# Kernel optimization log

Hardware: AMD Instinct MI355X
Metric: run time of the kernel (lower is better)

Reference implementation:

```python
import jax, jax.numpy as jnp
from jax import lax
import numpy as np

B, S, I, H = 128, 256, 1024, 1024


def setup_inputs() -> dict:
    key = jax.random.key(0)
    ks = jax.random.split(key, 9)
    scale = 1.0 / np.sqrt(I + H)  # ~ torch Linear default init scale
    mk_w = lambda k: jax.random.normal(k, (H, I + H), dtype=jnp.float32) * scale
    mk_b = lambda k: jax.random.normal(k, (H,), dtype=jnp.float32) * scale
    return {
        "x": jax.random.normal(ks[0], (B, S, I), dtype=jnp.float32),
        "Wf": mk_w(ks[1]), "bf": mk_b(ks[2]),
        "Wi": mk_w(ks[3]), "bi": mk_b(ks[4]),
        "Wc": mk_w(ks[5]), "bc": mk_b(ks[6]),
        "Wo": mk_w(ks[7]), "bo": mk_b(ks[8]),
    }


def reference(x, Wf, bf, Wi, bi, Wc, bc, Wo, bo):
    # x: [B, S, I]; weights: [H, I+H] acting on cat(h_t, x_t) (hidden first!)
    b, s, _ = x.shape
    h = Wf.shape[0]
    h0 = jnp.zeros((b, h), dtype=x.dtype)
    c0 = jnp.zeros((b, h), dtype=x.dtype)

    def step(carry, x_t):
        h_t, c_t = carry
        z = jnp.concatenate([h_t, x_t], axis=1)  # [B, H+I]
        f = jax.nn.sigmoid(z @ Wf.T + bf)
        i = jax.nn.sigmoid(z @ Wi.T + bi)
        g = jnp.tanh(z @ Wc.T + bc)
        c_new = c_t * f + i * g
        o = jax.nn.sigmoid(z @ Wo.T + bo)
        h_new = jnp.tanh(c_new) * o
        return (h_new, c_new), h_new

    _, hs = lax.scan(step, (h0, c0), jnp.swapaxes(x, 0, 1))  # hs: [S, B, H]
    return jnp.swapaxes(hs, 0, 1)  # [B, S, H]
```

## Files before the change

kernel.cpp:

```cpp
#include <hip/hip_runtime.h>
#include <stdint.h>


typedef unsigned short u16;
typedef unsigned int u32;
typedef __bf16 bf16x8 __attribute__((ext_vector_type(8)));
typedef float f32x4 __attribute__((ext_vector_type(4)));
typedef float f32x16 __attribute__((ext_vector_type(16)));

__device__ unsigned g_bars[128];
__device__ unsigned g_gxrdy[256];

__device__ __forceinline__ u16 f2bf(float f) {
  u32 u = __builtin_bit_cast(u32, f);
  u = (u + 0x7fffu + ((u >> 16) & 1u)) >> 16;
  return (u16)u;
}
__device__ __forceinline__ float bf2f(u16 s) {
  u32 u = ((u32)s) << 16;
  return __builtin_bit_cast(float, u);
}
__device__ __forceinline__ u32 pack2bf(float a, float b) {
  return (u32)f2bf(a) | ((u32)f2bf(b) << 16);
}

__device__ __forceinline__ void gl2lds16(const void* gptr, void* lptr) {
  __builtin_amdgcn_global_load_lds(
      (__attribute__((address_space(1))) void*)(uintptr_t)gptr,
      (__attribute__((address_space(3))) void*)(uintptr_t)lptr, 16, 0, 0);
}

__device__ __forceinline__ float sigm(float x) { return 1.f / (1.f + __expf(-x)); }
__device__ __forceinline__ float tanh_f(float x) { return 2.f / (1.f + __expf(-2.f * x)) - 1.f; }


__global__ __launch_bounds__(256) void convert_x(const float* __restrict__ x, u16* __restrict__ Xc) {
  int t = blockIdx.x * 256 + threadIdx.x;
  int i8 = t & 127;
  int s = (t >> 7) & 255;
  int b = t >> 15;
  const float4* src = (const float4*)(x + (((b << 8) + s) << 10) + (i8 << 3));
  float4 a = src[0], c = src[1];
  uint4 o;
  o.x = pack2bf(a.x, a.y); o.y = pack2bf(a.z, a.w);
  o.z = pack2bf(c.x, c.y); o.w = pack2bf(c.z, c.w);
  *(uint4*)(Xc + (((s << 7) + b) << 10) + (i8 << 3)) = o;
}

__global__ __launch_bounds__(256) void pack_w(const float* __restrict__ Wf, const float* __restrict__ Wi,
                                              const float* __restrict__ Wc, const float* __restrict__ Wo,
                                              u16* __restrict__ Whp, u16* __restrict__ Wxp) {
  int t = blockIdx.x * 256 + threadIdx.x;
  int k8 = t & 127, n = t >> 7;
  int g = n >> 10, h = n & 1023;
  const float* W = (g == 0) ? Wf : (g == 1) ? Wi : (g == 2) ? Wc : Wo;
  const float4* ph = (const float4*)(W + h * 2048 + (k8 << 3));
  float4 a = ph[0], b = ph[1];
  uint4 oh;
  oh.x = pack2bf(a.x, a.y); oh.y = pack2bf(a.z, a.w);
  oh.z = pack2bf(b.x, b.y); oh.w = pack2bf(b.z, b.w);
  *(uint4*)(Whp + n * 1024 + (k8 << 3)) = oh;
  const float4* px = (const float4*)(W + h * 2048 + 1024 + (k8 << 3));
  float4 c = px[0], d = px[1];
  uint4 ox;
  ox.x = pack2bf(c.x, c.y); ox.y = pack2bf(c.z, c.w);
  ox.z = pack2bf(d.x, d.y); ox.w = pack2bf(d.z, d.w);
  *(uint4*)(Wxp + n * 1024 + (k8 << 3)) = ox;
}

__global__ __launch_bounds__(256) void pack_b(const float* __restrict__ bf_, const float* __restrict__ bi,
                                              const float* __restrict__ bc, const float* __restrict__ bo,
                                              float* __restrict__ biasp) {
  if (blockIdx.x == 0 && threadIdx.x < 128) g_bars[threadIdx.x] = 0;
  if (blockIdx.x == 1) g_gxrdy[threadIdx.x] = 0;
  int n = blockIdx.x * 256 + threadIdx.x;
  int g = n >> 10, h = n & 1023;
  const float* b = (g == 0) ? bf_ : (g == 1) ? bi : (g == 2) ? bc : bo;
  biasp[n] = b[h];
}

__global__ __launch_bounds__(512, 2) void lstm_fused(
    const u16* __restrict__ Whp,
    const u16* __restrict__ Wxp,
    const u16* __restrict__ Xc,
    const float* __restrict__ biasp,
    u16* __restrict__ gx,
    u16* __restrict__ hring,
    float* __restrict__ cws,
    float* __restrict__ out) {
  __shared__ __align__(16) unsigned char smem[100352];
  const int tid = threadIdx.x;
  const int bid = blockIdx.x;

  if (bid >= 128) {
    u16* lds_a = (u16*)smem;
    u16* lds_b = (u16*)(smem + 32768);
    const int gid = bid - 128;
    const int lane = tid & 63, q = lane >> 4, cl = lane & 15;
    const int w = tid >> 6, wm = w & 1, wn = w >> 1;
    const int n0 = (gid & 31) * 128;

    for (int t = 0; t < 64; ++t) {
      const int s = (gid + (t << 7)) >> 5;
      const int m0 = s << 7;
      f32x4 acc[4][2] = {};

      auto stage = [&](int buf, int it) {
        const int k0 = it * 64;
#pragma unroll
        for (int itn = 0; itn < 2; ++itn) {
          int j = itn * 512 + tid;
          int row = j >> 3, c8s = (j & 7) ^ (row & 7);
          gl2lds16(Xc + (m0 + row) * 1024 + k0 + c8s * 8, lds_a + buf * 8192 + j * 8);
        }
#pragma unroll
        for (int itn = 0; itn < 2; ++itn) {
          int j = itn * 512 + tid;
          int row = j >> 3, c8s = (j & 7) ^ (row & 7);
          gl2lds16(Wxp + (n0 + row) * 1024 + k0 + c8s * 8, lds_b + buf * 8192 + j * 8);
        }
      };

      stage(0, 0);
      for (int it = 0; it < 16; ++it) {
        const int buf = it & 1;
        asm volatile("s_waitcnt vmcnt(0)" ::: "memory");
        __syncthreads();
        if (it < 15) stage(buf ^ 1, it + 1);
#pragma unroll
        for (int kk = 0; kk < 2; ++kk) {
          bf16x8 af[4], bfr[2];
#pragma unroll
          for (int mt = 0; mt < 4; ++mt) {
            int row = wm * 64 + mt * 16 + cl;
            int c8 = (kk * 4 + q) ^ (row & 7);
            af[mt] = *(const bf16x8*)&lds_a[buf * 8192 + row * 64 + c8 * 8];
          }
#pragma unroll
          for (int nt = 0; nt < 2; ++nt) {
            int row = wn * 32 + nt * 16 + cl;
            int c8 = (kk * 4 + q) ^ (row & 7);
            bfr[nt] = *(const bf16x8*)&lds_b[buf * 8192 + row * 64 + c8 * 8];
          }
#pragma unroll
          for (int mt = 0; mt < 4; ++mt)
#pragma unroll
            for (int nt = 0; nt < 2; ++nt)
              acc[mt][nt] = __builtin_amdgcn_mfma_f32_16x16x32_bf16(af[mt], bfr[nt], acc[mt][nt], 0, 0, 0);
        }
      }
#pragma unroll
      for (int nt = 0; nt < 2; ++nt) {
        int n = n0 + wn * 32 + nt * 16 + cl;
        float bv = biasp[n];
#pragma unroll
        for (int mt = 0; mt < 4; ++mt)
#pragma unroll
          for (int r = 0; r < 4; ++r) {
            int m = m0 + wm * 64 + mt * 16 + q * 4 + r;
            __hip_atomic_store(&gx[m * 4096 + n], f2bf(acc[mt][nt][r] + bv),
                               __ATOMIC_RELAXED, __HIP_MEMORY_SCOPE_AGENT);
          }
      }
      asm volatile("s_waitcnt vmcnt(0)" ::: "memory");
      __syncthreads();
      if (tid == 0)
        __hip_atomic_fetch_add(&g_gxrdy[s], 1u, __ATOMIC_RELAXED, __HIP_MEMORY_SCOPE_AGENT);
    }
    return;
  }

  u16* lds_h = (u16*)smem;
  float* pre = (float*)(smem + 65536);

  const int lane = tid & 63;
  const int w = tid >> 6;
  const int wn = w & 3;
  const int kh = w >> 2;
  const int l5 = lane >> 5, r31 = lane & 31;
  const int hgrp = bid & 31, mq = bid >> 5;
  const int h0 = hgrp * 32, m0 = mq * 32;
  unsigned* ctr = &g_bars[mq * 32];

  bf16x8 breg[32];
  {
    const int n_loc = wn * 32 + r31;
    const int ng = ((n_loc >> 5) << 10) + h0 + (n_loc & 31);
    const u16* wp = Whp + ng * 1024 + kh * 512 + l5 * 8;
#pragma unroll
    for (int ks = 0; ks < 32; ++ks) breg[ks] = *(const bf16x8*)(wp + ks * 16);
  }

  const int cm = tid >> 4, ch2 = (tid & 15) << 1;
  const int mg = m0 + cm;
  float2 cp = *(const float2*)&cws[mg * 1024 + h0 + ch2];
  float c0v = cp.x, c1v = cp.y;

  for (int s = 0; s < 256; ++s) {
    const u16* hin = hring + s * 131072;
    u16* hout = hring + (s + 1) * 131072;

    if (tid == 0) {
      while (__hip_atomic_load(&g_gxrdy[s], __ATOMIC_RELAXED, __HIP_MEMORY_SCOPE_AGENT) < 32u)
        __builtin_amdgcn_s_sleep(1);
      const unsigned tgt = 32u * (unsigned)s;
      while (__hip_atomic_load(ctr, __ATOMIC_RELAXED, __HIP_MEMORY_SCOPE_AGENT) < tgt)
        __builtin_amdgcn_s_sleep(1);
    }
    __syncthreads();

#pragma unroll
    for (int itn = 0; itn < 8; ++itn) {
      int j = itn * 512 + tid;
      int row = j >> 7, u = j & 127;
      int us = u ^ (row & 15);
      gl2lds16(hin + ((us >> 2) << 12) + ((m0 + row) << 5) + ((us & 3) << 3),
               lds_h + j * 8);
    }
    const int gbase = (s * 128 + mg) * 4096 + h0 + ch2;
    const u32 gq0 = *(const u32*)(gx + gbase);
    const u32 gq1 = *(const u32*)(gx + gbase + 1024);
    const u32 gq2 = *(const u32*)(gx + gbase + 2048);
    const u32 gq3 = *(const u32*)(gx + gbase + 3072);
    asm volatile("s_waitcnt vmcnt(0)" ::: "memory");
    __syncthreads();

    f32x16 acc0 = {}, acc1 = {};
#pragma unroll
    for (int ks = 0; ks < 32; ++ks) {
      const int g = kh * 64 + ks * 2 + l5;
      const bf16x8 av = *(const bf16x8*)&lds_h[r31 * 1024 + ((g ^ (r31 & 15)) << 3)];
      if (ks & 1)
        acc1 = __builtin_amdgcn_mfma_f32_32x32x16_bf16(av, breg[ks], acc1, 0, 0, 0);
      else
        acc0 = __builtin_amdgcn_mfma_f32_32x32x16_bf16(av, breg[ks], acc0, 0, 0, 0);
    }

#pragma unroll
    for (int r = 0; r < 16; ++r) {
      const int m_l = (r & 3) + ((r >> 2) << 3) + (l5 << 2);
      pre[(kh * 128 + wn * 32 + r31) * 34 + m_l] = acc0[r] + acc1[r];
    }
    __syncthreads();

    float p0[4], p1[4];
#pragma unroll
    for (int gi = 0; gi < 4; ++gi) {
      const int n0l = gi * 32 + ch2;
      p0[gi] = pre[n0l * 34 + cm] + pre[(128 + n0l) * 34 + cm];
      p1[gi] = pre[(n0l + 1) * 34 + cm] + pre[(128 + n0l + 1) * 34 + cm];
    }
    p0[0] += bf2f((u16)(gq0 & 0xffff)); p1[0] += bf2f((u16)(gq0 >> 16));
    p0[1] += bf2f((u16)(gq1 & 0xffff)); p1[1] += bf2f((u16)(gq1 >> 16));
    p0[2] += bf2f((u16)(gq2 & 0xffff)); p1[2] += bf2f((u16)(gq2 >> 16));
    p0[3] += bf2f((u16)(gq3 & 0xffff)); p1[3] += bf2f((u16)(gq3 >> 16));
    const float fg0 = sigm(p0[0]), ig0 = sigm(p0[1]), gg0 = tanh_f(p0[2]), og0 = sigm(p0[3]);
    const float fg1 = sigm(p1[0]), ig1 = sigm(p1[1]), gg1 = tanh_f(p1[2]), og1 = sigm(p1[3]);
    c0v = c0v * fg0 + ig0 * gg0;
    c1v = c1v * fg1 + ig1 * gg1;
    const float hn0 = tanh_f(c0v) * og0;
    const float hn1 = tanh_f(c1v) * og1;

    __hip_atomic_store((u32*)(hout + hgrp * 4096 + mg * 32 + ch2), pack2bf(hn0, hn1),
                       __ATOMIC_RELAXED, __HIP_MEMORY_SCOPE_AGENT);
    *(float2*)&out[(mg * 256 + s) * 1024 + h0 + ch2] = make_float2(hn0, hn1);

    asm volatile("s_waitcnt vmcnt(0)" ::: "memory");
    __syncthreads();
    if (tid == 0)
      __hip_atomic_fetch_add(ctr, 1u, __ATOMIC_RELAXED, __HIP_MEMORY_SCOPE_AGENT);
  }
  *(float2*)&cws[mg * 1024 + h0 + ch2] = make_float2(c0v, c1v);
}


extern "C" void kernel_launch(void* const* d_in, const int* in_sizes, int n_in,
                              void* d_out, int out_size, void* d_ws, size_t ws_size,
                              hipStream_t stream) {
  const float* x   = (const float*)d_in[0];
  const float* Wf  = (const float*)d_in[1];
  const float* bf_ = (const float*)d_in[2];
  const float* Wi  = (const float*)d_in[3];
  const float* bi  = (const float*)d_in[4];
  const float* Wc  = (const float*)d_in[5];
  const float* bc  = (const float*)d_in[6];
  const float* Wo  = (const float*)d_in[7];
  const float* bo  = (const float*)d_in[8];
  float* out = (float*)d_out;
  char* ws = (char*)d_ws;

  const size_t NEEDED = 420233216;
  if (ws_size < NEEDED) return;

  u16*  Xc    = (u16*)(ws);
  u16*  Whp   = (u16*)(ws + 67108864);
  u16*  Wxp   = (u16*)(ws + 75497472);
  float* biasp = (float*)(ws + 83886080);
  float* cws  = (float*)(ws + 83902464);
  u16*  hring = (u16*)(ws + 84426752);
  u16*  gx    = (u16*)(ws + 151797760);

  hipMemsetAsync(ws + 83902464, 0, 524288, stream);
  hipMemsetAsync(ws + 84426752, 0, 262144, stream);
  convert_x<<<16384, 256, 0, stream>>>(x, Xc);
  pack_w<<<2048, 256, 0, stream>>>(Wf, Wi, Wc, Wo, Whp, Wxp);
  pack_b<<<16, 256, 0, stream>>>(bf_, bi, bc, bo, biasp);

  void* args[8];
  args[0] = (void*)&Whp;
  args[1] = (void*)&Wxp;
  args[2] = (void*)&Xc;
  args[3] = (void*)&biasp;
  args[4] = (void*)&gx;
  args[5] = (void*)&hring;
  args[6] = (void*)&cws;
  args[7] = (void*)&out;
  if (hipLaunchCooperativeKernel((const void*)lstm_fused, dim3(256), dim3(512),
                                 args, 0, stream) != hipSuccess) {
    lstm_fused<<<dim3(256), dim3(512), 0, stream>>>(Whp, Wxp, Xc, biasp, gx, hring, cws, out);
  }
}
```

Baseline: 1.582 ms.

## Load h operand directly from global into registers, split K four ways

The recurrent blocks no longer stage the previous hidden state into LDS via global-to-LDS copies plus a barrier. Each wave now reads its MFMA A-operand fragments straight from the global h ring into registers, software-pipelined over 16 K-steps. The warps are reorganised into 2 N-halves by 4 K-quarters, so the cross-wave reduction in LDS grows to four partial sums. The fp32 output store is moved after the barrier arrival so it does not delay signalling the next step. This removes one LDS round trip and a __syncthreads per timestep, but relies on L2 latency for the operand loads and raises register pressure.

```diff
diff --git a/kernel.cpp b/kernel.cpp
--- a/kernel.cpp
+++ b/kernel.cpp
@@ -88,7 +88,7 @@
     u16* __restrict__ hring,
     float* __restrict__ cws,
     float* __restrict__ out) {
-  __shared__ __align__(16) unsigned char smem[100352];
+  __shared__ __align__(16) unsigned char smem[67584];
   const int tid = threadIdx.x;
   const int bid = blockIdx.x;
 
@@ -170,13 +170,12 @@
     return;
   }
 
-  u16* lds_h = (u16*)smem;
-  float* pre = (float*)(smem + 65536);
+  float* pre = (float*)smem;
 
   const int lane = tid & 63;
   const int w = tid >> 6;
-  const int wn = w & 3;
-  const int kh = w >> 2;
+  const int wn = w & 1;
+  const int kh = w >> 1;
   const int l5 = lane >> 5, r31 = lane & 31;
   const int hgrp = bid & 31, mq = bid >> 5;
   const int h0 = hgrp * 32, m0 = mq * 32;
@@ -184,12 +183,17 @@
 
   bf16x8 breg[32];
   {
-    const int n_loc = wn * 32 + r31;
-    const int ng = ((n_loc >> 5) << 10) + h0 + (n_loc & 31);
-    const u16* wp = Whp + ng * 1024 + kh * 512 + l5 * 8;
-#pragma unroll
-    for (int ks = 0; ks < 32; ++ks) breg[ks] = *(const bf16x8*)(wp + ks * 16);
+#pragma unroll
+    for (int nb = 0; nb < 2; ++nb) {
+      const int n_loc = wn * 64 + nb * 32 + r31;
+      const int ng = ((n_loc >> 5) << 10) + h0 + (n_loc & 31);
+      const u16* wp = Whp + ng * 1024 + kh * 256 + l5 * 8;
+#pragma unroll
+      for (int ks = 0; ks < 16; ++ks) breg[ks * 2 + nb] = *(const bf16x8*)(wp + ks * 16);
+    }
   }
+
+  const int voff = kh * 32768 + (m0 + r31) * 32 + l5 * 8;
 
   const int cm = tid >> 4, ch2 = (tid & 15) << 1;
   const int mg = m0 + cm;
@@ -197,7 +201,7 @@
   float c0v = cp.x, c1v = cp.y;
 
   for (int s = 0; s < 256; ++s) {
-    const u16* hin = hring + s * 131072;
+    const u16* hb = hring + s * 131072 + voff;
     u16* hout = hring + (s + 1) * 131072;
 
     if (tid == 0) {
@@ -209,37 +213,36 @@
     }
     __syncthreads();
 
-#pragma unroll
-    for (int itn = 0; itn < 8; ++itn) {
-      int j = itn * 512 + tid;
-      int row = j >> 7, u = j & 127;
-      int us = u ^ (row & 15);
-      gl2lds16(hin + ((us >> 2) << 12) + ((m0 + row) << 5) + ((us & 3) << 3),
-               lds_h + j * 8);
-    }
     const int gbase = (s * 128 + mg) * 4096 + h0 + ch2;
     const u32 gq0 = *(const u32*)(gx + gbase);
     const u32 gq1 = *(const u32*)(gx + gbase + 1024);
     const u32 gq2 = *(const u32*)(gx + gbase + 2048);
     const u32 gq3 = *(const u32*)(gx + gbase + 3072);
-    asm volatile("s_waitcnt vmcnt(0)" ::: "memory");
-    __syncthreads();
 
     f32x16 acc0 = {}, acc1 = {};
-#pragma unroll
-    for (int ks = 0; ks < 32; ++ks) {
-      const int g = kh * 64 + ks * 2 + l5;
-      const bf16x8 av = *(const bf16x8*)&lds_h[r31 * 1024 + ((g ^ (r31 & 15)) << 3)];
-      if (ks & 1)
-        acc1 = __builtin_amdgcn_mfma_f32_32x32x16_bf16(av, breg[ks], acc1, 0, 0, 0);
-      else
-        acc0 = __builtin_amdgcn_mfma_f32_32x32x16_bf16(av, breg[ks], acc0, 0, 0, 0);
+    bf16x8 av[8];
+#pragma unroll
+    for (int j = 0; j < 8; ++j)
+      av[j] = *(const bf16x8*)(hb + ((j >> 1) << 12) + ((j & 1) << 4));
+#pragma unroll
+    for (int j = 0; j < 8; ++j) {
+      const bf16x8 a = av[j];
+      const int ks = 8 + j;
+      av[j] = *(const bf16x8*)(hb + ((ks >> 1) << 12) + ((ks & 1) << 4));
+      acc0 = __builtin_amdgcn_mfma_f32_32x32x16_bf16(a, breg[2 * j], acc0, 0, 0, 0);
+      acc1 = __builtin_amdgcn_mfma_f32_32x32x16_bf16(a, breg[2 * j + 1], acc1, 0, 0, 0);
+    }
+#pragma unroll
+    for (int j = 0; j < 8; ++j) {
+      acc0 = __builtin_amdgcn_mfma_f32_32x32x16_bf16(av[j], breg[16 + 2 * j], acc0, 0, 0, 0);
+      acc1 = __builtin_amdgcn_mfma_f32_32x32x16_bf16(av[j], breg[17 + 2 * j], acc1, 0, 0, 0);
     }
 
 #pragma unroll
     for (int r = 0; r < 16; ++r) {
       const int m_l = (r & 3) + ((r >> 2) << 3) + (l5 << 2);
-      pre[(kh * 128 + wn * 32 + r31) * 34 + m_l] = acc0[r] + acc1[r];
+      pre[(kh * 128 + wn * 64 + r31) * 33 + m_l] = acc0[r];
+      pre[(kh * 128 + wn * 64 + 32 + r31) * 33 + m_l] = acc1[r];
     }
     __syncthreads();
 
@@ -247,8 +250,10 @@
 #pragma unroll
     for (int gi = 0; gi < 4; ++gi) {
       const int n0l = gi * 32 + ch2;
-      p0[gi] = pre[n0l * 34 + cm] + pre[(128 + n0l) * 34 + cm];
-      p1[gi] = pre[(n0l + 1) * 34 + cm] + pre[(128 + n0l + 1) * 34 + cm];
+      p0[gi] = pre[n0l * 33 + cm] + pre[(128 + n0l) * 33 + cm] +
+               pre[(256 + n0l) * 33 + cm] + pre[(384 + n0l) * 33 + cm];
+      p1[gi] = pre[(n0l + 1) * 33 + cm] + pre[(128 + n0l + 1) * 33 + cm] +
+               pre[(256 + n0l + 1) * 33 + cm] + pre[(384 + n0l + 1) * 33 + cm];
     }
     p0[0] += bf2f((u16)(gq0 & 0xffff)); p1[0] += bf2f((u16)(gq0 >> 16));
     p0[1] += bf2f((u16)(gq1 & 0xffff)); p1[1] += bf2f((u16)(gq1 >> 16));
@@ -263,12 +268,12 @@
 
     __hip_atomic_store((u32*)(hout + hgrp * 4096 + mg * 32 + ch2), pack2bf(hn0, hn1),
                        __ATOMIC_RELAXED, __HIP_MEMORY_SCOPE_AGENT);
-    *(float2*)&out[(mg * 256 + s) * 1024 + h0 + ch2] = make_float2(hn0, hn1);
-
     asm volatile("s_waitcnt vmcnt(0)" ::: "memory");
     __syncthreads();
     if (tid == 0)
       __hip_atomic_fetch_add(ctr, 1u, __ATOMIC_RELAXED, __HIP_MEMORY_SCOPE_AGENT);
+
+    *(float2*)&out[(mg * 256 + s) * 1024 + h0 + ch2] = make_float2(hn0, hn1);
   }
   *(float2*)&cws[mg * 1024 + h0 + ch2] = make_float2(c0v, c1v);
 }
```

Measured after the change: 1.576 ms. About the same (-0.4%).
